# Kernel optimization log

Hardware: AMD Instinct MI355X
Metric: run time of the kernel (lower is better)

Reference implementation:

```python
import math
import jax, jax.numpy as jnp
import numpy as np

LAMBDA_INIT = 0.8
GN_EPS = 1e-5

B, H, S, D = 2, 16, 2048, 128  # batch, heads, seq, head_dim


def setup_inputs() -> dict:
    key = jax.random.key(0)
    ks = jax.random.split(key, 8)
    return {
        "q": jax.random.normal(ks[0], (B, H, S, 2 * D), dtype=jnp.float32),
        "k": jax.random.normal(ks[1], (B, H, S, 2 * D), dtype=jnp.float32),
        "v": jax.random.normal(ks[2], (B, H, S, D), dtype=jnp.float32),
        "lam_q1": jax.random.normal(ks[3], (D,), dtype=jnp.float32),
        "lam_q2": jax.random.normal(ks[4], (D,), dtype=jnp.float32),
        "lam_k1": jax.random.normal(ks[5], (D,), dtype=jnp.float32),
        "lam_k2": jax.random.normal(ks[6], (D,), dtype=jnp.float32),
        "gn_weight": jnp.ones((H * D,), dtype=jnp.float32),
        "gn_bias": jnp.zeros((H * D,), dtype=jnp.float32),
    }


def reference(q, k, v, lam_q1, lam_q2, lam_k1, lam_k2, gn_weight, gn_bias):
    d = q.shape[-1] // 2
    scale = 1.0 / math.sqrt(d)
    Q1, Q2 = q[..., :d], q[..., d:]
    K1, K2 = k[..., :d], k[..., d:]
    # dual score matrices [B,H,S,S]
    w1 = jax.nn.softmax(jnp.einsum('bhsd,bhtd->bhst', Q1, K1) * scale, axis=-1)
    w2 = jax.nn.softmax(jnp.einsum('bhsd,bhtd->bhst', Q2, K2) * scale, axis=-1)
    lam = jnp.exp(jnp.dot(lam_q1, lam_k1)) - jnp.exp(jnp.dot(lam_q2, lam_k2)) + LAMBDA_INIT
    weights = w1 - lam * w2
    out = jnp.einsum('bhst,bhtd->bhsd', weights, v)  # [B,H,S,D]
    # GroupNorm(num_groups=H, num_channels=H*D) applied on [B, H*D, S]:
    # channel c = h*D + dd, normalization per (batch, head) over (D, S).
    mean = out.mean(axis=(2, 3), keepdims=True)
    var = out.var(axis=(2, 3), keepdims=True)
    normed = (out - mean) * jax.lax.rsqrt(var + GN_EPS)
    gamma = gn_weight.reshape(1, out.shape[1], 1, d)
    beta = gn_bias.reshape(1, out.shape[1], 1, d)
    return (normed * gamma + beta) * (1.0 - LAMBDA_INIT)
```

## Files before the change

### kernel.cpp

```cpp
#include <hip/hip_runtime.h>
#include <cstddef>

constexpr int B = 2, H = 16, S = 2048, D = 128;
constexpr int BH = B * H;
constexpr int TWOD = 2 * D;
constexpr int QTILE = 128;
constexpr int BC = 32;
constexpr int NKT = S / BC;
constexpr float SC2 = 0.08838834764831845f * 1.4426950408889634f;
constexpr float LAM_INIT = 0.8f;
constexpr float GN_EPS = 1e-5f;

typedef __attribute__((ext_vector_type(8))) short short8;
typedef __attribute__((ext_vector_type(4))) float f32x4;

__device__ __forceinline__ unsigned short f2b(float f) {
  unsigned int u = __float_as_uint(f);
  u += 0x7fffu + ((u >> 16) & 1u);
  return (unsigned short)(u >> 16);
}

__device__ __forceinline__ void async_copy16(const void* g, void* l) {
  typedef __attribute__((address_space(1))) const void gvoid;
  typedef __attribute__((address_space(3))) void lvoid;
  __builtin_amdgcn_global_load_lds((gvoid*)g, (lvoid*)l, 16, 0, 0);
}

__global__ void convk_kernel(const float* __restrict__ src, unsigned short* __restrict__ dst,
                             const float* __restrict__ lq1, const float* __restrict__ lq2,
                             const float* __restrict__ lk1, const float* __restrict__ lk2,
                             float* __restrict__ wsf) {
  if (blockIdx.x == 0 && threadIdx.x < 64) {
    int t = threadIdx.x;
    float s1 = lq1[t] * lk1[t] + lq1[t + 64] * lk1[t + 64];
    float s2 = lq2[t] * lk2[t] + lq2[t + 64] * lk2[t + 64];
#pragma unroll
    for (int off = 32; off >= 1; off >>= 1) {
      s1 += __shfl_xor(s1, off, 64);
      s2 += __shfl_xor(s2, off, 64);
    }
    if (t == 0) wsf[0] = expf(s1) - expf(s2) + LAM_INIT;
  }
  size_t i = ((size_t)blockIdx.x * 256 + threadIdx.x) * 8;
  float4 a = *(const float4*)(src + i);
  float4 b = *(const float4*)(src + i + 4);
  unsigned short u[8];
  u[0] = f2b(a.x); u[1] = f2b(a.y); u[2] = f2b(a.z); u[3] = f2b(a.w);
  u[4] = f2b(b.x); u[5] = f2b(b.y); u[6] = f2b(b.z); u[7] = f2b(b.w);
  *(uint4*)(dst + i) = *(uint4*)u;
}

__global__ void vt_kernel(const float* __restrict__ v, unsigned short* __restrict__ vtg) {
  __shared__ float tile[64][129];
  const int bh = blockIdx.y, s0 = blockIdx.x * 64, t = threadIdx.x;
#pragma unroll
  for (int i = 0; i < 8; ++i) {
    int idx = t + i * 256;
    int row = idx >> 5, c4 = idx & 31;
    float4 f = *(const float4*)(v + ((size_t)bh * S + s0 + row) * D + c4 * 4);
    tile[row][c4 * 4 + 0] = f.x; tile[row][c4 * 4 + 1] = f.y;
    tile[row][c4 * 4 + 2] = f.z; tile[row][c4 * 4 + 3] = f.w;
  }
  __syncthreads();
#pragma unroll
  for (int i = 0; i < 4; ++i) {
    int c = t + i * 256;
    int d = c >> 3, k8 = c & 7;
    unsigned short u[8];
#pragma unroll
    for (int j = 0; j < 8; ++j) u[j] = f2b(tile[k8 * 8 + j][d]);
    *(uint4*)(vtg + ((size_t)bh * D + d) * S + s0 + k8 * 8) = *(uint4*)u;
  }
}

__global__ __launch_bounds__(256, 2)
void attn_kernel(const float* __restrict__ q, const unsigned short* __restrict__ kbf,
                 const unsigned short* __restrict__ vtg,
                 float* __restrict__ wsf, float* __restrict__ out) {
  __shared__ __attribute__((aligned(16))) unsigned short Ks[2][32][256];
  __shared__ __attribute__((aligned(16))) unsigned short Vt[2][128][40];
  __shared__ __attribute__((aligned(16))) unsigned short Pa[4][2][32][40];
  __shared__ float sred[4][2];

  const int bh = blockIdx.x, qb = blockIdx.y;
  const int q0 = qb * QTILE;
  const int tid = threadIdx.x;
  const int wave = tid >> 6, lane = tid & 63;
  const int quad = lane >> 4, l16 = lane & 15;
  const float lam = wsf[0];

  short8 qf[2][2][4];
#pragma unroll
  for (int mt = 0; mt < 2; ++mt) {
    int qrow = q0 + wave * 32 + mt * 16 + l16;
    const float* qr = q + ((size_t)bh * S + qrow) * TWOD;
#pragma unroll
    for (int st = 0; st < 2; ++st)
#pragma unroll
      for (int ks = 0; ks < 4; ++ks) {
        const float* p = qr + st * D + ks * 32 + quad * 8;
        float4 f0 = *(const float4*)p;
        float4 f1 = *(const float4*)(p + 4);
        short8 v8;
        v8[0] = (short)f2b(f0.x * SC2); v8[1] = (short)f2b(f0.y * SC2);
        v8[2] = (short)f2b(f0.z * SC2); v8[3] = (short)f2b(f0.w * SC2);
        v8[4] = (short)f2b(f1.x * SC2); v8[5] = (short)f2b(f1.y * SC2);
        v8[6] = (short)f2b(f1.z * SC2); v8[7] = (short)f2b(f1.w * SC2);
        qf[mt][st][ks] = v8;
      }
  }

  const unsigned short* kbase = kbf + (size_t)bh * S * (size_t)TWOD;
  int goff[4];
#pragma unroll
  for (int i = 0; i < 4; ++i) {
    int L = i * 256 + tid;
    int row = L >> 5, cp = L & 31;
    int g = cp ^ (row & 7);
    goff[i] = row * 256 + g * 8;
  }
  const unsigned short* vbase = vtg + (size_t)bh * D * (size_t)S;
  const int vd0 = tid >> 2, vcp = tid & 3;

  f32x4 acc[2][2][8];
#pragma unroll
  for (int mt = 0; mt < 2; ++mt)
#pragma unroll
    for (int st = 0; st < 2; ++st)
#pragma unroll
      for (int n = 0; n < 8; ++n) acc[mt][st][n] = (f32x4){0.f, 0.f, 0.f, 0.f};
  float lacc[2][2];
#pragma unroll
  for (int mt = 0; mt < 2; ++mt)
#pragma unroll
    for (int st = 0; st < 2; ++st) lacc[mt][st] = 0.f;

  auto qk = [&](int st, int kb, f32x4 (&sa)[2][2]) {
#pragma unroll
    for (int nt = 0; nt < 2; ++nt) {
      const int row = nt * 16 + l16;
      const int rx = row & 7;
#pragma unroll
      for (int ks = 0; ks < 4; ++ks) {
        const int pos = (st * 16 + ks * 4 + quad) ^ rx;
        const short8 kf = *(const short8*)&Ks[kb][row][pos * 8];
        sa[0][nt] = __builtin_amdgcn_mfma_f32_16x16x32_bf16(kf, qf[0][st][ks], sa[0][nt], 0, 0, 0);
        sa[1][nt] = __builtin_amdgcn_mfma_f32_16x16x32_bf16(kf, qf[1][st][ks], sa[1][nt], 0, 0, 0);
      }
    }
  };
  auto pexp = [&](int st, f32x4 (&sa)[2][2]) {
#pragma unroll
    for (int mt = 0; mt < 2; ++mt)
#pragma unroll
      for (int nt = 0; nt < 2; ++nt) {
        float p0 = __builtin_amdgcn_exp2f(sa[mt][nt][0]);
        float p1 = __builtin_amdgcn_exp2f(sa[mt][nt][1]);
        float p2 = __builtin_amdgcn_exp2f(sa[mt][nt][2]);
        float p3 = __builtin_amdgcn_exp2f(sa[mt][nt][3]);
        lacc[mt][st] += (p0 + p1) + (p2 + p3);
        uint2 w;
        w.x = (unsigned int)f2b(p0) | ((unsigned int)f2b(p1) << 16);
        w.y = (unsigned int)f2b(p2) | ((unsigned int)f2b(p3) << 16);
        *(uint2*)&Pa[wave][st][mt * 16 + l16][nt * 16 + quad * 4] = w;
      }
  };
  auto pv = [&](int st, const short8 (&paf)[2], const short8 (&vf)[8]) {
#pragma unroll
    for (int nt8 = 0; nt8 < 8; ++nt8)
#pragma unroll
      for (int mt = 0; mt < 2; ++mt)
        acc[mt][st][nt8] = __builtin_amdgcn_mfma_f32_16x16x32_bf16(paf[mt], vf[nt8], acc[mt][st][nt8], 0, 0, 0);
  };

  {
    const uint4 z = {0u, 0u, 0u, 0u};
    unsigned short* pz = &Pa[0][0][0][0];
    for (int i = tid; i < 1280; i += 256) *(uint4*)(pz + i * 8) = z;
    unsigned short* vz = &Vt[1][0][0];
    for (int i = tid; i < 640; i += 256) *(uint4*)(vz + i * 8) = z;
#pragma unroll
    for (int i = 0; i < 4; ++i)
      async_copy16(kbase + goff[i], &Ks[0][0][0] + (i * 256 + tid) * 8);
    uint4 v0 = *(const uint4*)(vbase + (size_t)vd0 * S + vcp * 8);
    uint4 v1 = *(const uint4*)(vbase + (size_t)(vd0 + 64) * S + vcp * 8);
    *(uint4*)&Vt[0][vd0][vcp * 8] = v0;
    *(uint4*)&Vt[0][vd0 + 64][vcp * 8] = v1;
  }
  __syncthreads();

  for (int t = 0; t < NKT; ++t) {
    const int kbuf = t & 1;
    const int pvbuf = kbuf ^ 1;

    short8 paf[2][2], vf[8];
#pragma unroll
    for (int st = 0; st < 2; ++st)
#pragma unroll
      for (int mt = 0; mt < 2; ++mt)
        paf[st][mt] = *(const short8*)&Pa[wave][st][mt * 16 + l16][quad * 8];
#pragma unroll
    for (int nt8 = 0; nt8 < 8; ++nt8)
      vf[nt8] = *(const short8*)&Vt[pvbuf][nt8 * 16 + l16][quad * 8];

    const bool pre = (t + 1 < NKT);
    uint4 vr0, vr1;
    if (pre) {
      const unsigned short* vp = vbase + (t + 1) * BC + vcp * 8;
      vr0 = *(const uint4*)(vp + (size_t)vd0 * S);
      vr1 = *(const uint4*)(vp + (size_t)(vd0 + 64) * S);
      const unsigned short* kp = kbase + (size_t)(t + 1) * BC * TWOD;
      unsigned short* ldsb = &Ks[pvbuf][0][0];
#pragma unroll
      for (int i = 0; i < 4; ++i)
        async_copy16(kp + goff[i], ldsb + (i * 256 + tid) * 8);
    }

    f32x4 sa0[2][2], sa1[2][2];
#pragma unroll
    for (int mt = 0; mt < 2; ++mt)
#pragma unroll
      for (int nt = 0; nt < 2; ++nt) {
        sa0[mt][nt] = (f32x4){0.f, 0.f, 0.f, 0.f};
        sa1[mt][nt] = (f32x4){0.f, 0.f, 0.f, 0.f};
      }
    qk(0, kbuf, sa0);
    pv(0, paf[0], vf);
    pexp(0, sa0);
    qk(1, kbuf, sa1);
    pv(1, paf[1], vf);
    pexp(1, sa1);

    __syncthreads();
    if (pre) {
      *(uint4*)&Vt[pvbuf][vd0][vcp * 8] = vr0;
      *(uint4*)&Vt[pvbuf][vd0 + 64][vcp * 8] = vr1;
    }
  }

  {
    short8 paf[2][2], vf[8];
#pragma unroll
    for (int st = 0; st < 2; ++st)
#pragma unroll
      for (int mt = 0; mt < 2; ++mt)
        paf[st][mt] = *(const short8*)&Pa[wave][st][mt * 16 + l16][quad * 8];
#pragma unroll
    for (int nt8 = 0; nt8 < 8; ++nt8)
      vf[nt8] = *(const short8*)&Vt[1][nt8 * 16 + l16][quad * 8];
    pv(0, paf[0], vf);
    pv(1, paf[1], vf);
  }

#pragma unroll
  for (int mt = 0; mt < 2; ++mt)
#pragma unroll
    for (int st = 0; st < 2; ++st) {
      float v = lacc[mt][st];
      v += __shfl_xor(v, 16, 64);
      v += __shfl_xor(v, 32, 64);
      lacc[mt][st] = v;
    }

  float sum = 0.f, ssq = 0.f;
#pragma unroll
  for (int mt = 0; mt < 2; ++mt) {
    float i1[4], i2[4];
#pragma unroll
    for (int r = 0; r < 4; ++r) {
      i1[r] = 1.f / __shfl(lacc[mt][0], quad * 4 + r, 64);
      i2[r] = lam / __shfl(lacc[mt][1], quad * 4 + r, 64);
    }
#pragma unroll
    for (int nt8 = 0; nt8 < 8; ++nt8)
#pragma unroll
      for (int r = 0; r < 4; ++r) {
        float o = acc[mt][0][nt8][r] * i1[r] - acc[mt][1][nt8][r] * i2[r];
        int row = q0 + wave * 32 + mt * 16 + quad * 4 + r;
        out[((size_t)bh * S + row) * D + nt8 * 16 + l16] = o;
        sum += o; ssq += o * o;
      }
  }
#pragma unroll
  for (int off = 32; off >= 1; off >>= 1) {
    sum += __shfl_xor(sum, off, 64);
    ssq += __shfl_xor(ssq, off, 64);
  }
  if (lane == 0) { sred[wave][0] = sum; sred[wave][1] = ssq; }
  __syncthreads();
  if (tid == 0) {
    float s0 = sred[0][0] + sred[1][0] + sred[2][0] + sred[3][0];
    float s1 = sred[0][1] + sred[1][1] + sred[2][1] + sred[3][1];
    int idx = bh * 16 + qb;
    wsf[64 + idx * 2] = s0;
    wsf[64 + idx * 2 + 1] = s1;
  }
}

__global__ void gn_kernel(float* __restrict__ out, const float* __restrict__ gw,
                          const float* __restrict__ gb, const float* __restrict__ wsf) {
  const int bh = blockIdx.x, part = blockIdx.y;
  const int h = bh & (H - 1);
  float sum = 0.f, ssq = 0.f;
  for (int j = 0; j < 16; ++j) {
    sum += wsf[64 + (bh * 16 + j) * 2];
    ssq += wsf[64 + (bh * 16 + j) * 2 + 1];
  }
  const float invn = 1.f / (float)(S * D);
  const float mean = sum * invn;
  const float var = ssq * invn - mean * mean;
  const float rstd = rsqrtf(var + GN_EPS);
  const float outscale = 1.f - LAM_INIT;
  const float4* g4 = (const float4*)(gw + h * D);
  const float4* b4 = (const float4*)(gb + h * D);
  float4* o4 = (float4*)(out + (size_t)bh * S * D);
  const int chunks_per = (S * D / 4) / 8;
  const int c0 = part * chunks_per;
  for (int c = c0 + threadIdx.x; c < c0 + chunks_per; c += 256) {
    float4 vv = o4[c];
    int d4 = c & 31;
    float4 g = g4[d4], bb = b4[d4];
    vv.x = ((vv.x - mean) * rstd * g.x + bb.x) * outscale;
    vv.y = ((vv.y - mean) * rstd * g.y + bb.y) * outscale;
    vv.z = ((vv.z - mean) * rstd * g.z + bb.z) * outscale;
    vv.w = ((vv.w - mean) * rstd * g.w + bb.w) * outscale;
    o4[c] = vv;
  }
}

extern "C" void kernel_launch(void* const* d_in, const int* in_sizes, int n_in,
                              void* d_out, int out_size, void* d_ws, size_t ws_size,
                              hipStream_t stream) {
  (void)in_sizes; (void)n_in; (void)out_size; (void)ws_size;
  const float* q   = (const float*)d_in[0];
  const float* k   = (const float*)d_in[1];
  const float* v   = (const float*)d_in[2];
  const float* lq1 = (const float*)d_in[3];
  const float* lq2 = (const float*)d_in[4];
  const float* lk1 = (const float*)d_in[5];
  const float* lk2 = (const float*)d_in[6];
  const float* gw  = (const float*)d_in[7];
  const float* gb  = (const float*)d_in[8];
  float* out = (float*)d_out;
  float* wsf = (float*)d_ws;
  unsigned short* vtg = (unsigned short*)((char*)d_ws + 8192);
  unsigned short* kbf = (unsigned short*)((char*)d_ws + 8192 + (size_t)BH * D * S * 2);

  convk_kernel<<<dim3(BH * S * TWOD / 2048), dim3(256), 0, stream>>>(k, kbf, lq1, lq2, lk1, lk2, wsf);
  vt_kernel<<<dim3(S / 64, BH), dim3(256), 0, stream>>>(v, vtg);
  attn_kernel<<<dim3(BH, S / QTILE), dim3(256), 0, stream>>>(q, kbf, vtg, wsf, out);
  gn_kernel<<<dim3(BH, 8), dim3(256), 0, stream>>>(out, gw, gb, wsf);
}
```

Measured before the change: 385.6 us.

## Split dual-softmax streams across waves and redistribute P via shuffles

Halves the query tile and assigns each wave pair to one of the two score streams (Q1K1 or Q2K2), so each wave holds half the accumulators. The P matrix is passed from the QK layout to the PV operand layout through lane shuffles instead of a round trip through shared memory. The two streams are combined at the end through a shared-memory buffer that aliases the K buffers. Grid size doubles, occupancy target rises to 3 blocks, and the GroupNorm partial-sum indexing and workspace offsets change to match. In exchange, each block reloads the full K/V stream for half as many queries, which doubles global K/V traffic.

```diff
diff --git a/kernel.cpp b/kernel.cpp
--- a/kernel.cpp
+++ b/kernel.cpp
@@ -4,7 +4,7 @@
 constexpr int B = 2, H = 16, S = 2048, D = 128;
 constexpr int BH = B * H;
 constexpr int TWOD = 2 * D;
-constexpr int QTILE = 128;
+constexpr int QTILE = 64;
 constexpr int BC = 32;
 constexpr int NKT = S / BC;
 constexpr float SC2 = 0.08838834764831845f * 1.4426950408889634f;
@@ -73,41 +73,41 @@
   }
 }
 
-__global__ __launch_bounds__(256, 2)
+__global__ __launch_bounds__(256, 3)
 void attn_kernel(const float* __restrict__ q, const unsigned short* __restrict__ kbf,
                  const unsigned short* __restrict__ vtg,
                  float* __restrict__ wsf, float* __restrict__ out) {
-  __shared__ __attribute__((aligned(16))) unsigned short Ks[2][32][256];
-  __shared__ __attribute__((aligned(16))) unsigned short Vt[2][128][40];
-  __shared__ __attribute__((aligned(16))) unsigned short Pa[4][2][32][40];
-  __shared__ float sred[4][2];
+  __shared__ __attribute__((aligned(16))) unsigned char smem_raw[53248];
+  __shared__ float sred[2][2];
+  unsigned short (*Ks)[32][256] = (unsigned short (*)[32][256])smem_raw;
+  unsigned short (*Vt)[128][40] = (unsigned short (*)[128][40])(smem_raw + 32768);
+  float (*Ob)[132] = (float (*)[132])smem_raw;
 
   const int bh = blockIdx.x, qb = blockIdx.y;
   const int q0 = qb * QTILE;
   const int tid = threadIdx.x;
   const int wave = tid >> 6, lane = tid & 63;
+  const int st = wave & 1, wq = wave >> 1;
   const int quad = lane >> 4, l16 = lane & 15;
   const float lam = wsf[0];
 
-  short8 qf[2][2][4];
+  short8 qf[2][4];
 #pragma unroll
   for (int mt = 0; mt < 2; ++mt) {
-    int qrow = q0 + wave * 32 + mt * 16 + l16;
-    const float* qr = q + ((size_t)bh * S + qrow) * TWOD;
-#pragma unroll
-    for (int st = 0; st < 2; ++st)
-#pragma unroll
-      for (int ks = 0; ks < 4; ++ks) {
-        const float* p = qr + st * D + ks * 32 + quad * 8;
-        float4 f0 = *(const float4*)p;
-        float4 f1 = *(const float4*)(p + 4);
-        short8 v8;
-        v8[0] = (short)f2b(f0.x * SC2); v8[1] = (short)f2b(f0.y * SC2);
-        v8[2] = (short)f2b(f0.z * SC2); v8[3] = (short)f2b(f0.w * SC2);
-        v8[4] = (short)f2b(f1.x * SC2); v8[5] = (short)f2b(f1.y * SC2);
-        v8[6] = (short)f2b(f1.z * SC2); v8[7] = (short)f2b(f1.w * SC2);
-        qf[mt][st][ks] = v8;
-      }
+    int qrow = q0 + wq * 32 + mt * 16 + l16;
+    const float* qr = q + ((size_t)bh * S + qrow) * TWOD + st * D;
+#pragma unroll
+    for (int ks = 0; ks < 4; ++ks) {
+      const float* p = qr + ks * 32 + quad * 8;
+      float4 f0 = *(const float4*)p;
+      float4 f1 = *(const float4*)(p + 4);
+      short8 v8;
+      v8[0] = (short)f2b(f0.x * SC2); v8[1] = (short)f2b(f0.y * SC2);
+      v8[2] = (short)f2b(f0.z * SC2); v8[3] = (short)f2b(f0.w * SC2);
+      v8[4] = (short)f2b(f1.x * SC2); v8[5] = (short)f2b(f1.y * SC2);
+      v8[6] = (short)f2b(f1.z * SC2); v8[7] = (short)f2b(f1.w * SC2);
+      qf[mt][ks] = v8;
+    }
   }
 
   const unsigned short* kbase = kbf + (size_t)bh * S * (size_t)TWOD;
@@ -122,61 +122,77 @@
   const unsigned short* vbase = vtg + (size_t)bh * D * (size_t)S;
   const int vd0 = tid >> 2, vcp = tid & 3;
 
-  f32x4 acc[2][2][8];
+  f32x4 acc[2][8];
 #pragma unroll
   for (int mt = 0; mt < 2; ++mt)
 #pragma unroll
-    for (int st = 0; st < 2; ++st)
-#pragma unroll
-      for (int n = 0; n < 8; ++n) acc[mt][st][n] = (f32x4){0.f, 0.f, 0.f, 0.f};
-  float lacc[2][2];
-#pragma unroll
-  for (int mt = 0; mt < 2; ++mt)
-#pragma unroll
-    for (int st = 0; st < 2; ++st) lacc[mt][st] = 0.f;
-
-  auto qk = [&](int st, int kb, f32x4 (&sa)[2][2]) {
+    for (int n = 0; n < 8; ++n) acc[mt][n] = (f32x4){0.f, 0.f, 0.f, 0.f};
+  float lacc[2] = {0.f, 0.f};
+
+  short8 pa[2];
+  {
+    uint4 z4 = {0u, 0u, 0u, 0u};
+    pa[0] = *(short8*)&z4; pa[1] = *(short8*)&z4;
+  }
+  const int stq = st * 16;
+  const int srcA = ((quad * 2) & 3) * 16 + l16;
+  const int srcB = ((quad * 2 + 1) & 3) * 16 + l16;
+  const bool hi = quad >= 2;
+
+  auto qk = [&](int kb, f32x4 (&sa)[2][2]) {
 #pragma unroll
     for (int nt = 0; nt < 2; ++nt) {
       const int row = nt * 16 + l16;
       const int rx = row & 7;
 #pragma unroll
       for (int ks = 0; ks < 4; ++ks) {
-        const int pos = (st * 16 + ks * 4 + quad) ^ rx;
+        const int pos = (stq + ks * 4 + quad) ^ rx;
         const short8 kf = *(const short8*)&Ks[kb][row][pos * 8];
-        sa[0][nt] = __builtin_amdgcn_mfma_f32_16x16x32_bf16(kf, qf[0][st][ks], sa[0][nt], 0, 0, 0);
-        sa[1][nt] = __builtin_amdgcn_mfma_f32_16x16x32_bf16(kf, qf[1][st][ks], sa[1][nt], 0, 0, 0);
+        sa[0][nt] = __builtin_amdgcn_mfma_f32_16x16x32_bf16(kf, qf[0][ks], sa[0][nt], 0, 0, 0);
+        sa[1][nt] = __builtin_amdgcn_mfma_f32_16x16x32_bf16(kf, qf[1][ks], sa[1][nt], 0, 0, 0);
       }
     }
   };
-  auto pexp = [&](int st, f32x4 (&sa)[2][2]) {
-#pragma unroll
-    for (int mt = 0; mt < 2; ++mt)
+  auto pexp_redist = [&](f32x4 (&sa)[2][2]) {
+#pragma unroll
+    for (int mt = 0; mt < 2; ++mt) {
+      unsigned int w[2][2];
 #pragma unroll
       for (int nt = 0; nt < 2; ++nt) {
         float p0 = __builtin_amdgcn_exp2f(sa[mt][nt][0]);
         float p1 = __builtin_amdgcn_exp2f(sa[mt][nt][1]);
         float p2 = __builtin_amdgcn_exp2f(sa[mt][nt][2]);
         float p3 = __builtin_amdgcn_exp2f(sa[mt][nt][3]);
-        lacc[mt][st] += (p0 + p1) + (p2 + p3);
-        uint2 w;
-        w.x = (unsigned int)f2b(p0) | ((unsigned int)f2b(p1) << 16);
-        w.y = (unsigned int)f2b(p2) | ((unsigned int)f2b(p3) << 16);
-        *(uint2*)&Pa[wave][st][mt * 16 + l16][nt * 16 + quad * 4] = w;
+        lacc[mt] += (p0 + p1) + (p2 + p3);
+        w[nt][0] = (unsigned int)f2b(p0) | ((unsigned int)f2b(p1) << 16);
+        w[nt][1] = (unsigned int)f2b(p2) | ((unsigned int)f2b(p3) << 16);
       }
+      unsigned int a0 = (unsigned int)__shfl((int)w[0][0], srcA, 64);
+      unsigned int a1 = (unsigned int)__shfl((int)w[0][1], srcA, 64);
+      unsigned int a2 = (unsigned int)__shfl((int)w[0][0], srcB, 64);
+      unsigned int a3 = (unsigned int)__shfl((int)w[0][1], srcB, 64);
+      unsigned int b0 = (unsigned int)__shfl((int)w[1][0], srcA, 64);
+      unsigned int b1 = (unsigned int)__shfl((int)w[1][1], srcA, 64);
+      unsigned int b2 = (unsigned int)__shfl((int)w[1][0], srcB, 64);
+      unsigned int b3 = (unsigned int)__shfl((int)w[1][1], srcB, 64);
+      uint4 pu;
+      pu.x = hi ? b0 : a0;
+      pu.y = hi ? b1 : a1;
+      pu.z = hi ? b2 : a2;
+      pu.w = hi ? b3 : a3;
+      pa[mt] = *(short8*)&pu;
+    }
   };
-  auto pv = [&](int st, const short8 (&paf)[2], const short8 (&vf)[8]) {
+  auto pv = [&](const short8 (&vf)[8]) {
 #pragma unroll
     for (int nt8 = 0; nt8 < 8; ++nt8)
 #pragma unroll
       for (int mt = 0; mt < 2; ++mt)
-        acc[mt][st][nt8] = __builtin_amdgcn_mfma_f32_16x16x32_bf16(paf[mt], vf[nt8], acc[mt][st][nt8], 0, 0, 0);
+        acc[mt][nt8] = __builtin_amdgcn_mfma_f32_16x16x32_bf16(pa[mt], vf[nt8], acc[mt][nt8], 0, 0, 0);
   };
 
   {
     const uint4 z = {0u, 0u, 0u, 0u};
-    unsigned short* pz = &Pa[0][0][0][0];
-    for (int i = tid; i < 1280; i += 256) *(uint4*)(pz + i * 8) = z;
     unsigned short* vz = &Vt[1][0][0];
     for (int i = tid; i < 640; i += 256) *(uint4*)(vz + i * 8) = z;
 #pragma unroll
@@ -193,12 +209,7 @@
     const int kbuf = t & 1;
     const int pvbuf = kbuf ^ 1;
 
-    short8 paf[2][2], vf[8];
-#pragma unroll
-    for (int st = 0; st < 2; ++st)
-#pragma unroll
-      for (int mt = 0; mt < 2; ++mt)
-        paf[st][mt] = *(const short8*)&Pa[wave][st][mt * 16 + l16][quad * 8];
+    short8 vf[8];
 #pragma unroll
     for (int nt8 = 0; nt8 < 8; ++nt8)
       vf[nt8] = *(const short8*)&Vt[pvbuf][nt8 * 16 + l16][quad * 8];
@@ -216,20 +227,14 @@
         async_copy16(kp + goff[i], ldsb + (i * 256 + tid) * 8);
     }
 
-    f32x4 sa0[2][2], sa1[2][2];
+    f32x4 sa[2][2];
 #pragma unroll
     for (int mt = 0; mt < 2; ++mt)
 #pragma unroll
-      for (int nt = 0; nt < 2; ++nt) {
-        sa0[mt][nt] = (f32x4){0.f, 0.f, 0.f, 0.f};
-        sa1[mt][nt] = (f32x4){0.f, 0.f, 0.f, 0.f};
-      }
-    qk(0, kbuf, sa0);
-    pv(0, paf[0], vf);
-    pexp(0, sa0);
-    qk(1, kbuf, sa1);
-    pv(1, paf[1], vf);
-    pexp(1, sa1);
+      for (int nt = 0; nt < 2; ++nt) sa[mt][nt] = (f32x4){0.f, 0.f, 0.f, 0.f};
+    qk(kbuf, sa);
+    pv(vf);
+    pexp_redist(sa);
 
     __syncthreads();
     if (pre) {
@@ -239,59 +244,66 @@
   }
 
   {
-    short8 paf[2][2], vf[8];
-#pragma unroll
-    for (int st = 0; st < 2; ++st)
-#pragma unroll
-      for (int mt = 0; mt < 2; ++mt)
-        paf[st][mt] = *(const short8*)&Pa[wave][st][mt * 16 + l16][quad * 8];
+    short8 vf[8];
 #pragma unroll
     for (int nt8 = 0; nt8 < 8; ++nt8)
       vf[nt8] = *(const short8*)&Vt[1][nt8 * 16 + l16][quad * 8];
-    pv(0, paf[0], vf);
-    pv(1, paf[1], vf);
-  }
-
-#pragma unroll
-  for (int mt = 0; mt < 2; ++mt)
-#pragma unroll
-    for (int st = 0; st < 2; ++st) {
-      float v = lacc[mt][st];
-      v += __shfl_xor(v, 16, 64);
-      v += __shfl_xor(v, 32, 64);
-      lacc[mt][st] = v;
-    }
-
-  float sum = 0.f, ssq = 0.f;
+    pv(vf);
+  }
+
 #pragma unroll
   for (int mt = 0; mt < 2; ++mt) {
-    float i1[4], i2[4];
-#pragma unroll
-    for (int r = 0; r < 4; ++r) {
-      i1[r] = 1.f / __shfl(lacc[mt][0], quad * 4 + r, 64);
-      i2[r] = lam / __shfl(lacc[mt][1], quad * 4 + r, 64);
-    }
-#pragma unroll
-    for (int nt8 = 0; nt8 < 8; ++nt8)
-#pragma unroll
-      for (int r = 0; r < 4; ++r) {
-        float o = acc[mt][0][nt8][r] * i1[r] - acc[mt][1][nt8][r] * i2[r];
-        int row = q0 + wave * 32 + mt * 16 + quad * 4 + r;
-        out[((size_t)bh * S + row) * D + nt8 * 16 + l16] = o;
-        sum += o; ssq += o * o;
-      }
-  }
-#pragma unroll
-  for (int off = 32; off >= 1; off >>= 1) {
-    sum += __shfl_xor(sum, off, 64);
-    ssq += __shfl_xor(ssq, off, 64);
-  }
-  if (lane == 0) { sred[wave][0] = sum; sred[wave][1] = ssq; }
+    float v = lacc[mt];
+    v += __shfl_xor(v, 16, 64);
+    v += __shfl_xor(v, 32, 64);
+    lacc[mt] = v;
+  }
+
+  const int obase = wq * 32;
+  if (st == 1) {
+#pragma unroll
+    for (int mt = 0; mt < 2; ++mt) {
+      float i2[4];
+#pragma unroll
+      for (int r = 0; r < 4; ++r) i2[r] = lam / __shfl(lacc[mt], quad * 4 + r, 64);
+#pragma unroll
+      for (int nt8 = 0; nt8 < 8; ++nt8)
+#pragma unroll
+        for (int r = 0; r < 4; ++r)
+          Ob[obase + mt * 16 + quad * 4 + r][nt8 * 16 + l16] = acc[mt][nt8][r] * i2[r];
+    }
+  }
+  __syncthreads();
+  if (st == 0) {
+    float sum = 0.f, ssq = 0.f;
+#pragma unroll
+    for (int mt = 0; mt < 2; ++mt) {
+      float i1[4];
+#pragma unroll
+      for (int r = 0; r < 4; ++r) i1[r] = 1.f / __shfl(lacc[mt], quad * 4 + r, 64);
+#pragma unroll
+      for (int nt8 = 0; nt8 < 8; ++nt8)
+#pragma unroll
+        for (int r = 0; r < 4; ++r) {
+          float o = acc[mt][nt8][r] * i1[r]
+                  - Ob[obase + mt * 16 + quad * 4 + r][nt8 * 16 + l16];
+          int row = q0 + obase + mt * 16 + quad * 4 + r;
+          out[((size_t)bh * S + row) * D + nt8 * 16 + l16] = o;
+          sum += o; ssq += o * o;
+        }
+    }
+#pragma unroll
+    for (int off = 32; off >= 1; off >>= 1) {
+      sum += __shfl_xor(sum, off, 64);
+      ssq += __shfl_xor(ssq, off, 64);
+    }
+    if (lane == 0) { sred[wq][0] = sum; sred[wq][1] = ssq; }
+  }
   __syncthreads();
   if (tid == 0) {
-    float s0 = sred[0][0] + sred[1][0] + sred[2][0] + sred[3][0];
-    float s1 = sred[0][1] + sred[1][1] + sred[2][1] + sred[3][1];
-    int idx = bh * 16 + qb;
+    float s0 = sred[0][0] + sred[1][0];
+    float s1 = sred[0][1] + sred[1][1];
+    int idx = bh * 32 + qb;
     wsf[64 + idx * 2] = s0;
     wsf[64 + idx * 2 + 1] = s1;
   }
@@ -302,9 +314,9 @@
   const int bh = blockIdx.x, part = blockIdx.y;
   const int h = bh & (H - 1);
   float sum = 0.f, ssq = 0.f;
-  for (int j = 0; j < 16; ++j) {
-    sum += wsf[64 + (bh * 16 + j) * 2];
-    ssq += wsf[64 + (bh * 16 + j) * 2 + 1];
+  for (int j = 0; j < 32; ++j) {
+    sum += wsf[64 + (bh * 32 + j) * 2];
+    ssq += wsf[64 + (bh * 32 + j) * 2 + 1];
   }
   const float invn = 1.f / (float)(S * D);
   const float mean = sum * invn;
@@ -343,8 +355,8 @@
   const float* gb  = (const float*)d_in[8];
   float* out = (float*)d_out;
   float* wsf = (float*)d_ws;
-  unsigned short* vtg = (unsigned short*)((char*)d_ws + 8192);
-  unsigned short* kbf = (unsigned short*)((char*)d_ws + 8192 + (size_t)BH * D * S * 2);
+  unsigned short* vtg = (unsigned short*)((char*)d_ws + 16384);
+  unsigned short* kbf = (unsigned short*)((char*)d_ws + 16384 + (size_t)BH * D * S * 2);
 
   convk_kernel<<<dim3(BH * S * TWOD / 2048), dim3(256), 0, stream>>>(k, kbf, lq1, lq2, lk1, lk2, wsf);
   vt_kernel<<<dim3(S / 64, BH), dim3(256), 0, stream>>>(v, vtg);
```

New measurement: 397.2 us. 1.03x slower.
